# Kernel tuning notes

Hardware: AMD Instinct MI355X
Metric: run time of the kernel (lower is better)

## Reference

```python
import jax, jax.numpy as jnp
from jax import lax
import numpy as np

WINDOW_SIZE = 11
SIGMA = 1.5
C1 = 0.01 ** 2
C2 = 0.03 ** 2


def _gauss_1d(n=WINDOW_SIZE, sigma=SIGMA):
    # replicates cv2.getGaussianKernel(n, sigma)
    x = np.arange(n, dtype=np.float64) - (n - 1) / 2.0
    g = np.exp(-(x ** 2) / (2.0 * sigma ** 2))
    return (g / g.sum()).astype(np.float32)


def _blur(x, g):
    """Separable 2D Gaussian blur of x [N,1,H,W]; math equals conv with g g^T."""
    p = g.shape[0] // 2
    kh = g.reshape(1, 1, -1, 1).astype(x.dtype)  # [O,I,KH,1]
    kw = g.reshape(1, 1, 1, -1).astype(x.dtype)  # [O,I,1,KW]
    dn = ('NCHW', 'OIHW', 'NCHW')
    x = lax.conv_general_dilated(x, kh, (1, 1), [(p, p), (0, 0)], dimension_numbers=dn)
    x = lax.conv_general_dilated(x, kw, (1, 1), [(0, 0), (p, p)], dimension_numbers=dn)
    return x


def _ssim_loss_2d(a, b):
    """a, b: [N,1,H,W]. Returns 1 - mean(SSIM map) with the module's exact formula."""
    g = jnp.asarray(_gauss_1d())
    mu1 = _blur(a, g)
    mu2 = _blur(b, g)
    mu1_sq = mu1 * mu1
    mu2_sq = mu2 * mu2
    mu1_mu2 = mu1 * mu2
    sigma1_sq = _blur(a * a, g) - mu1_sq
    sigma2_sq = _blur(b * b, g) - mu2_sq
    sigma12 = _blur(a * b, g) - mu1_mu2
    luminance = (2 * mu1_mu2 + C1) / (mu1_sq + mu2_sq + C1)
    contrast = (2 * sigma12 + C2) / (sigma1_sq + sigma2_sq + C2)
    structure = (sigma12 + C2) / (jnp.sqrt(sigma1_sq) * jnp.sqrt(sigma2_sq) + C2)
    ssim = luminance * contrast * structure
    return 1.0 - ssim.mean()


def setup_inputs() -> dict:
    key = jax.random.key(0)
    k1, k2, k3 = jax.random.split(key, 3)
    img1_3d = jax.random.uniform(k1, (4, 1, 16, 512, 512), dtype=jnp.float32)
    img1_2d = jax.random.uniform(k2, (4, 1, 512, 512), dtype=jnp.float32)
    img2 = jax.random.uniform(k3, (4, 1, 16, 512, 512), dtype=jnp.float32)
    return {"img1_3d": img1_3d, "img1_2d": img1_2d, "img2": img2}


def reference(img1_3d, img1_2d, img2):
    B, C, D, H, W = img1_3d.shape  # C == 1 (forced by groups=C with single-out-channel weight)
    # 3D SSIM: kernel depth 1, depth padding 0 -> per-slice 2D blur; fold D into batch.
    a3 = img1_3d.reshape(B * D, 1, H, W)
    b3 = img2.reshape(B * D, 1, H, W)
    loss3d = _ssim_loss_2d(a3, b3)
    # 2D SSIM against depth-averaged img2.
    b2 = jnp.mean(img2, axis=2)  # [B,1,H,W]
    loss2d = _ssim_loss_2d(img1_2d, b2)
    return loss3d + loss2d
```

## Files before the change

kernel.cpp:

```cpp
#include <hip/hip_runtime.h>
#include <cmath>


#define WSZ 11
#define IMG 512
#define SLICE (IMG * IMG)

typedef float f32x2 __attribute__((ext_vector_type(2)));
typedef float f32x4 __attribute__((ext_vector_type(4)));

struct G11 { float w[WSZ]; };

__device__ __forceinline__ void row_barrier()
{
    asm volatile("s_waitcnt lgkmcnt(0)" ::: "memory");
    __builtin_amdgcn_s_barrier();
}

__global__ __launch_bounds__(256, 5)
void ssim_pk_kernel(const float* __restrict__ A3, const float* __restrict__ B3,
                    const float* __restrict__ A2, const float* __restrict__ B2,
                    double* __restrict__ acc, G11 gw)
{
    __shared__ f32x4 A4[2][262];
    __shared__ f32x4 B4[2][262];
    __shared__ f32x2 Z2[2][262];
    __shared__ float bsum[4];

    const int tx = threadIdx.x;
    const int x0 = tx * 2;

    const int unit = blockIdx.x;
    const float* Ap;
    const float* Bp;
    double* accp;
    int y0, TST;
    if (unit < 1536) {
        int slice = unit / 24;
        int band  = unit - slice * 24;
        Ap = A3 + (long)slice * SLICE;
        Bp = B3 + (long)slice * SLICE;
        accp = acc + 0;
        if (band < 16) { y0 = band * 22;              TST = 22 + 10; }
        else           { y0 = 352 + (band - 16) * 20; TST = 20 + 10; }
    } else {
        int uu = unit - 1536;
        int img  = uu >> 6;
        int band = uu & 63;
        Ap = A2 + (long)img * SLICE;
        Bp = B2 + (long)img * SLICE;
        accp = acc + 1;
        y0 = band * 8;
        TST = 8 + 10;
    }

    if (tx < 3) {
        f32x4 z4 = {0.f, 0.f, 0.f, 0.f};
        f32x2 z2 = {0.f, 0.f};
        A4[0][tx] = z4; A4[1][tx] = z4; A4[0][259 + tx] = z4; A4[1][259 + tx] = z4;
        B4[0][tx] = z4; B4[1][tx] = z4; B4[0][259 + tx] = z4; B4[1][259 + tx] = z4;
        Z2[0][tx] = z2; Z2[1][tx] = z2; Z2[0][259 + tx] = z2; Z2[1][259 + tx] = z2;
    }

    f32x2 ra[11], rb[11];
    #pragma unroll
    for (int i = 0; i < 11; i++) { ra[i] = (f32x2){0.f, 0.f}; rb[i] = (f32x2){0.f, 0.f}; }

    float sum = 0.f;

    f32x2 aN = {0.f, 0.f}, bN = {0.f, 0.f};
    {
        int r = y0 - 5;
        if (r >= 0 && r < IMG) {
            aN = *(const f32x2*)&Ap[(long)r * IMG + x0];
            bN = *(const f32x2*)&Bp[(long)r * IMG + x0];
        }
    }

    const f32x2 C1v = {1e-4f, 1e-4f};
    const f32x2 C2v = {9e-4f, 9e-4f};

    for (int t0 = 0; t0 < TST; t0 += 11) {
        #pragma unroll
        for (int u = 0; u < 11; u++) {
            const int t = t0 + u;
            if (t < TST) {
                ra[u] = aN;
                rb[u] = bN;

                {
                    int rn = y0 - 4 + t;
                    aN = (f32x2){0.f, 0.f}; bN = (f32x2){0.f, 0.f};
                    if ((t + 1 < TST) && rn >= 0 && rn < IMG) {
                        aN = *(const f32x2*)&Ap[(long)rn * IMG + x0];
                        bN = *(const f32x2*)&Bp[(long)rn * IMG + x0];
                    }
                }

                if (t >= 10) {
                    f32x2 m1 = {0.f, 0.f}, m2 = m1, xx = m1, yy = m1, zz = m1;
                    #pragma unroll
                    for (int j = 0; j < 11; j++) {
                        const int s = (u + 1 + j) % 11;
                        const f32x2 g2 = {gw.w[j], gw.w[j]};
                        f32x2 a = ra[s], b = rb[s];
                        f32x2 ga = g2 * a, gb = g2 * b;
                        m1 += ga; m2 += gb;
                        xx += ga * a; yy += gb * b; zz += ga * b;
                    }
                    const int buf = t & 1;
                    A4[buf][3 + tx] = __builtin_shufflevector(m1, m2, 0, 1, 2, 3);
                    B4[buf][3 + tx] = __builtin_shufflevector(xx, yy, 0, 1, 2, 3);
                    Z2[buf][3 + tx] = zz;
                    row_barrier();

                    f32x2 OM1 = {0.f, 0.f}, OM2 = OM1, OXX = OM1, OYY = OM1, OZZ = OM1;
                    {
                        f32x4 pa = A4[buf][tx], pb = B4[buf][tx];
                        f32x2 pz = Z2[buf][tx];
                        const f32x2 c = {gw.w[0], 0.f};
                        OM1 += c * __builtin_shufflevector(pa, pa, 1, 1);
                        OM2 += c * __builtin_shufflevector(pa, pa, 3, 3);
                        OXX += c * __builtin_shufflevector(pb, pb, 1, 1);
                        OYY += c * __builtin_shufflevector(pb, pb, 3, 3);
                        OZZ += c * __builtin_shufflevector(pz, pz, 1, 1);
                    }
                    #pragma unroll
                    for (int jj = 1; jj <= 5; jj++) {
                        f32x4 pa = A4[buf][tx + jj], pb = B4[buf][tx + jj];
                        f32x2 pz = Z2[buf][tx + jj];
                        const f32x2 cA = {gw.w[2 * jj - 1], gw.w[2 * jj - 2]};
                        const f32x2 cB = {gw.w[2 * jj],     gw.w[2 * jj - 1]};
                        OM1 += cA * __builtin_shufflevector(pa, pa, 0, 0)
                             + cB * __builtin_shufflevector(pa, pa, 1, 1);
                        OM2 += cA * __builtin_shufflevector(pa, pa, 2, 2)
                             + cB * __builtin_shufflevector(pa, pa, 3, 3);
                        OXX += cA * __builtin_shufflevector(pb, pb, 0, 0)
                             + cB * __builtin_shufflevector(pb, pb, 1, 1);
                        OYY += cA * __builtin_shufflevector(pb, pb, 2, 2)
                             + cB * __builtin_shufflevector(pb, pb, 3, 3);
                        OZZ += cA * __builtin_shufflevector(pz, pz, 0, 0)
                             + cB * __builtin_shufflevector(pz, pz, 1, 1);
                    }
                    {
                        f32x4 pa = A4[buf][tx + 6], pb = B4[buf][tx + 6];
                        f32x2 pz = Z2[buf][tx + 6];
                        const f32x2 c = {0.f, gw.w[10]};
                        OM1 += c * __builtin_shufflevector(pa, pa, 0, 0);
                        OM2 += c * __builtin_shufflevector(pa, pa, 2, 2);
                        OXX += c * __builtin_shufflevector(pb, pb, 0, 0);
                        OYY += c * __builtin_shufflevector(pb, pb, 2, 2);
                        OZZ += c * __builtin_shufflevector(pz, pz, 0, 0);
                    }

                    f32x2 m1s = OM1 * OM1, m2s = OM2 * OM2, m12 = OM1 * OM2;
                    f32x2 s1 = OXX - m1s, s2 = OYY - m2s, s12 = OZZ - m12;
                    f32x2 d1 = m1s + m2s + C1v;
                    f32x2 d2 = s1 + s2 + C2v;
                    f32x2 num = (2.f * m12 + C1v) * (2.f * s12 + C2v) * (s12 + C2v);
                    float d3x = __builtin_amdgcn_sqrtf(s1.x) * __builtin_amdgcn_sqrtf(s2.x) + 9e-4f;
                    float d3y = __builtin_amdgcn_sqrtf(s1.y) * __builtin_amdgcn_sqrtf(s2.y) + 9e-4f;
                    sum += num.x * __builtin_amdgcn_rcpf(d1.x * d2.x * d3x);
                    sum += num.y * __builtin_amdgcn_rcpf(d1.y * d2.y * d3y);
                }
            }
        }
    }

    for (int off = 32; off > 0; off >>= 1)
        sum += __shfl_down(sum, off, 64);
    if ((tx & 63) == 0) bsum[tx >> 6] = sum;
    __syncthreads();
    if (tx == 0) {
        float tot = bsum[0] + bsum[1] + bsum[2] + bsum[3];
        atomicAdd(accp, (double)tot);
    }
}

__global__ __launch_bounds__(256) void depth_mean4_kernel(
    const float4* __restrict__ img2, float4* __restrict__ b2)
{
    const int per = SLICE / 4;
    int idx = blockIdx.x * 256 + threadIdx.x;
    int b = idx >> 16;
    int p = idx & (per - 1);
    const float4* src = img2 + (long)b * 16 * per + p;
    float sx = 0.f, sy = 0.f, sz = 0.f, sw = 0.f;
    #pragma unroll
    for (int d = 0; d < 16; d++) {
        float4 v = src[(long)d * per];
        sx += v.x; sy += v.y; sz += v.z; sw += v.w;
    }
    float4 o; o.x = sx * 0.0625f; o.y = sy * 0.0625f; o.z = sz * 0.0625f; o.w = sw * 0.0625f;
    b2[idx] = o;
}

__global__ void finalize_kernel(const double* __restrict__ acc, float* __restrict__ out)
{
    double loss3 = 1.0 - acc[0] / (64.0 * (double)SLICE);
    double loss2 = 1.0 - acc[1] / (4.0 * (double)SLICE);
    out[0] = (float)(loss3 + loss2);
}

extern "C" void kernel_launch(void* const* d_in, const int* in_sizes, int n_in,
                              void* d_out, int out_size, void* d_ws, size_t ws_size,
                              hipStream_t stream)
{
    const float* img1_3d = (const float*)d_in[0];
    const float* img1_2d = (const float*)d_in[1];
    const float* img2    = (const float*)d_in[2];
    float* out = (float*)d_out;

    double* acc = (double*)d_ws;
    float*  b2  = (float*)((char*)d_ws + 256);

    G11 gw;
    {
        double g[WSZ], s = 0.0;
        for (int i = 0; i < WSZ; i++) {
            double xx = (double)i - (WSZ - 1) / 2.0;
            g[i] = std::exp(-(xx * xx) / (2.0 * 1.5 * 1.5));
            s += g[i];
        }
        for (int i = 0; i < WSZ; i++) gw.w[i] = (float)(g[i] / s);
    }

    hipMemsetAsync(acc, 0, 2 * sizeof(double), stream);

    depth_mean4_kernel<<<(4 * SLICE / 4) / 256, 256, 0, stream>>>(
        (const float4*)img2, (float4*)b2);

    ssim_pk_kernel<<<1792, 256, 0, stream>>>(img1_3d, img2, img1_2d, b2, acc, gw);

    finalize_kernel<<<1, 1, 0, stream>>>(acc, out);
}
```

Before: 105.4 us.

## Process two output rows per barrier with a 12-slot ring and quad LDS buffers

Restructures the sliding-window loop so each iteration loads two new input rows, computes two vertical blur passes into separate LDS buffers, and then does a single barrier before two horizontal passes. The register ring grows from 11 to 12 entries, the LDS staging goes from double to quad buffering, and the warm-up now loads the first 10 rows up front instead of looping through them with predicated compute. The goal is to halve the number of workgroup barriers per output row and to keep more loads in flight. In exchange it uses more registers and LDS, and the occupancy hint drops from 5 to 4 waves.

After: 93.98 us, median of 2. 1.12x faster.

```diff
diff --git a/kernel.cpp b/kernel.cpp
--- a/kernel.cpp
+++ b/kernel.cpp
@@ -17,14 +17,14 @@
     __builtin_amdgcn_s_barrier();
 }
 
-__global__ __launch_bounds__(256, 5)
+__global__ __launch_bounds__(256, 4)
 void ssim_pk_kernel(const float* __restrict__ A3, const float* __restrict__ B3,
                     const float* __restrict__ A2, const float* __restrict__ B2,
                     double* __restrict__ acc, G11 gw)
 {
-    __shared__ f32x4 A4[2][262];
-    __shared__ f32x4 B4[2][262];
-    __shared__ f32x2 Z2[2][262];
+    __shared__ f32x4 A4[4][262];
+    __shared__ f32x4 B4[4][262];
+    __shared__ f32x2 Z2[4][262];
     __shared__ float bsum[4];
 
     const int tx = threadIdx.x;
@@ -34,15 +34,15 @@
     const float* Ap;
     const float* Bp;
     double* accp;
-    int y0, TST;
+    int y0, BAND;
     if (unit < 1536) {
         int slice = unit / 24;
         int band  = unit - slice * 24;
         Ap = A3 + (long)slice * SLICE;
         Bp = B3 + (long)slice * SLICE;
         accp = acc + 0;
-        if (band < 16) { y0 = band * 22;              TST = 22 + 10; }
-        else           { y0 = 352 + (band - 16) * 20; TST = 20 + 10; }
+        if (band < 16) { y0 = band * 22;              BAND = 22; }
+        else           { y0 = 352 + (band - 16) * 20; BAND = 20; }
     } else {
         int uu = unit - 1536;
         int img  = uu >> 6;
@@ -51,118 +51,142 @@
         Bp = B2 + (long)img * SLICE;
         accp = acc + 1;
         y0 = band * 8;
-        TST = 8 + 10;
-    }
+        BAND = 8;
+    }
+    const int ITER = BAND >> 1;
 
     if (tx < 3) {
         f32x4 z4 = {0.f, 0.f, 0.f, 0.f};
         f32x2 z2 = {0.f, 0.f};
-        A4[0][tx] = z4; A4[1][tx] = z4; A4[0][259 + tx] = z4; A4[1][259 + tx] = z4;
-        B4[0][tx] = z4; B4[1][tx] = z4; B4[0][259 + tx] = z4; B4[1][259 + tx] = z4;
-        Z2[0][tx] = z2; Z2[1][tx] = z2; Z2[0][259 + tx] = z2; Z2[1][259 + tx] = z2;
-    }
-
-    f32x2 ra[11], rb[11];
-    #pragma unroll
-    for (int i = 0; i < 11; i++) { ra[i] = (f32x2){0.f, 0.f}; rb[i] = (f32x2){0.f, 0.f}; }
+        #pragma unroll
+        for (int b = 0; b < 4; b++) {
+            A4[b][tx] = z4; A4[b][259 + tx] = z4;
+            B4[b][tx] = z4; B4[b][259 + tx] = z4;
+            Z2[b][tx] = z2; Z2[b][259 + tx] = z2;
+        }
+    }
+
+    f32x2 ra[12], rb[12];
 
     float sum = 0.f;
-
-    f32x2 aN = {0.f, 0.f}, bN = {0.f, 0.f};
-    {
-        int r = y0 - 5;
-        if (r >= 0 && r < IMG) {
-            aN = *(const f32x2*)&Ap[(long)r * IMG + x0];
-            bN = *(const f32x2*)&Bp[(long)r * IMG + x0];
-        }
-    }
-
     const f32x2 C1v = {1e-4f, 1e-4f};
     const f32x2 C2v = {9e-4f, 9e-4f};
 
-    for (int t0 = 0; t0 < TST; t0 += 11) {
-        #pragma unroll
-        for (int u = 0; u < 11; u++) {
-            const int t = t0 + u;
-            if (t < TST) {
-                ra[u] = aN;
-                rb[u] = bN;
+    #pragma unroll
+    for (int t = 0; t < 10; t++) {
+        int r = y0 - 5 + t;
+        f32x2 a = {0.f, 0.f}, b = {0.f, 0.f};
+        if (r >= 0) {
+            a = *(const f32x2*)&Ap[(long)r * IMG + x0];
+            b = *(const f32x2*)&Bp[(long)r * IMG + x0];
+        }
+        ra[t] = a; rb[t] = b;
+    }
+    ra[10] = (f32x2){0.f, 0.f}; rb[10] = (f32x2){0.f, 0.f};
+    ra[11] = (f32x2){0.f, 0.f}; rb[11] = (f32x2){0.f, 0.f};
+
+    f32x2 aN0 = {0.f, 0.f}, bN0 = aN0, aN1 = aN0, bN1 = aN0;
+    {
+        int r0 = y0 + 5, r1 = y0 + 6;
+        if (r0 < IMG) { aN0 = *(const f32x2*)&Ap[(long)r0 * IMG + x0];
+                        bN0 = *(const f32x2*)&Bp[(long)r0 * IMG + x0]; }
+        if (r1 < IMG) { aN1 = *(const f32x2*)&Ap[(long)r1 * IMG + x0];
+                        bN1 = *(const f32x2*)&Bp[(long)r1 * IMG + x0]; }
+    }
+
+    auto vpass = [&](int base, int buf) {
+        f32x2 m1 = {0.f, 0.f}, m2 = m1, xx = m1, yy = m1, zz = m1;
+        #pragma unroll
+        for (int j = 0; j < 11; j++) {
+            const int s = (base + j) % 12;
+            const f32x2 g2 = {gw.w[j], gw.w[j]};
+            f32x2 a = ra[s], b = rb[s];
+            f32x2 ga = g2 * a, gb = g2 * b;
+            m1 += ga; m2 += gb;
+            xx += ga * a; yy += gb * b; zz += ga * b;
+        }
+        A4[buf][3 + tx] = __builtin_shufflevector(m1, m2, 0, 1, 2, 3);
+        B4[buf][3 + tx] = __builtin_shufflevector(xx, yy, 0, 1, 2, 3);
+        Z2[buf][3 + tx] = zz;
+    };
+
+    auto hpass = [&](int buf) {
+        f32x2 OM1 = {0.f, 0.f}, OM2 = OM1, OXX = OM1, OYY = OM1, OZZ = OM1;
+        {
+            f32x4 pa = A4[buf][tx], pb = B4[buf][tx];
+            f32x2 pz = Z2[buf][tx];
+            const f32x2 c = {gw.w[0], 0.f};
+            OM1 += c * __builtin_shufflevector(pa, pa, 1, 1);
+            OM2 += c * __builtin_shufflevector(pa, pa, 3, 3);
+            OXX += c * __builtin_shufflevector(pb, pb, 1, 1);
+            OYY += c * __builtin_shufflevector(pb, pb, 3, 3);
+            OZZ += c * __builtin_shufflevector(pz, pz, 1, 1);
+        }
+        #pragma unroll
+        for (int jj = 1; jj <= 5; jj++) {
+            f32x4 pa = A4[buf][tx + jj], pb = B4[buf][tx + jj];
+            f32x2 pz = Z2[buf][tx + jj];
+            const f32x2 cA = {gw.w[2 * jj - 1], gw.w[2 * jj - 2]};
+            const f32x2 cB = {gw.w[2 * jj],     gw.w[2 * jj - 1]};
+            OM1 += cA * __builtin_shufflevector(pa, pa, 0, 0)
+                 + cB * __builtin_shufflevector(pa, pa, 1, 1);
+            OM2 += cA * __builtin_shufflevector(pa, pa, 2, 2)
+                 + cB * __builtin_shufflevector(pa, pa, 3, 3);
+            OXX += cA * __builtin_shufflevector(pb, pb, 0, 0)
+                 + cB * __builtin_shufflevector(pb, pb, 1, 1);
+            OYY += cA * __builtin_shufflevector(pb, pb, 2, 2)
+                 + cB * __builtin_shufflevector(pb, pb, 3, 3);
+            OZZ += cA * __builtin_shufflevector(pz, pz, 0, 0)
+                 + cB * __builtin_shufflevector(pz, pz, 1, 1);
+        }
+        {
+            f32x4 pa = A4[buf][tx + 6], pb = B4[buf][tx + 6];
+            f32x2 pz = Z2[buf][tx + 6];
+            const f32x2 c = {0.f, gw.w[10]};
+            OM1 += c * __builtin_shufflevector(pa, pa, 0, 0);
+            OM2 += c * __builtin_shufflevector(pa, pa, 2, 2);
+            OXX += c * __builtin_shufflevector(pb, pb, 0, 0);
+            OYY += c * __builtin_shufflevector(pb, pb, 2, 2);
+            OZZ += c * __builtin_shufflevector(pz, pz, 0, 0);
+        }
+        f32x2 m1s = OM1 * OM1, m2s = OM2 * OM2, m12 = OM1 * OM2;
+        f32x2 s1 = OXX - m1s, s2 = OYY - m2s, s12 = OZZ - m12;
+        f32x2 d1 = m1s + m2s + C1v;
+        f32x2 d2 = s1 + s2 + C2v;
+        f32x2 num = (2.f * m12 + C1v) * (2.f * s12 + C2v) * (s12 + C2v);
+        float d3x = __builtin_amdgcn_sqrtf(s1.x) * __builtin_amdgcn_sqrtf(s2.x) + 9e-4f;
+        float d3y = __builtin_amdgcn_sqrtf(s1.y) * __builtin_amdgcn_sqrtf(s2.y) + 9e-4f;
+        sum += num.x * __builtin_amdgcn_rcpf(d1.x * d2.x * d3x);
+        sum += num.y * __builtin_amdgcn_rcpf(d1.y * d2.y * d3y);
+    };
+
+    for (int kk = 0; kk < ITER; kk += 6) {
+        #pragma unroll
+        for (int u = 0; u < 6; u++) {
+            const int k = kk + u;
+            if (k < ITER) {
+                const int s0 = (10 + 2 * u) % 12;
+                const int s1 = (11 + 2 * u) % 12;
+                ra[s0] = aN0; rb[s0] = bN0;
+                ra[s1] = aN1; rb[s1] = bN1;
 
                 {
-                    int rn = y0 - 4 + t;
-                    aN = (f32x2){0.f, 0.f}; bN = (f32x2){0.f, 0.f};
-                    if ((t + 1 < TST) && rn >= 0 && rn < IMG) {
-                        aN = *(const f32x2*)&Ap[(long)rn * IMG + x0];
-                        bN = *(const f32x2*)&Bp[(long)rn * IMG + x0];
+                    int r0 = y0 + 7 + 2 * k, r1 = r0 + 1;
+                    aN0 = (f32x2){0.f, 0.f}; bN0 = aN0; aN1 = aN0; bN1 = aN0;
+                    if (k + 1 < ITER) {
+                        if (r0 < IMG) { aN0 = *(const f32x2*)&Ap[(long)r0 * IMG + x0];
+                                        bN0 = *(const f32x2*)&Bp[(long)r0 * IMG + x0]; }
+                        if (r1 < IMG) { aN1 = *(const f32x2*)&Ap[(long)r1 * IMG + x0];
+                                        bN1 = *(const f32x2*)&Bp[(long)r1 * IMG + x0]; }
                     }
                 }
 
-                if (t >= 10) {
-                    f32x2 m1 = {0.f, 0.f}, m2 = m1, xx = m1, yy = m1, zz = m1;
-                    #pragma unroll
-                    for (int j = 0; j < 11; j++) {
-                        const int s = (u + 1 + j) % 11;
-                        const f32x2 g2 = {gw.w[j], gw.w[j]};
-                        f32x2 a = ra[s], b = rb[s];
-                        f32x2 ga = g2 * a, gb = g2 * b;
-                        m1 += ga; m2 += gb;
-                        xx += ga * a; yy += gb * b; zz += ga * b;
-                    }
-                    const int buf = t & 1;
-                    A4[buf][3 + tx] = __builtin_shufflevector(m1, m2, 0, 1, 2, 3);
-                    B4[buf][3 + tx] = __builtin_shufflevector(xx, yy, 0, 1, 2, 3);
-                    Z2[buf][3 + tx] = zz;
-                    row_barrier();
-
-                    f32x2 OM1 = {0.f, 0.f}, OM2 = OM1, OXX = OM1, OYY = OM1, OZZ = OM1;
-                    {
-                        f32x4 pa = A4[buf][tx], pb = B4[buf][tx];
-                        f32x2 pz = Z2[buf][tx];
-                        const f32x2 c = {gw.w[0], 0.f};
-                        OM1 += c * __builtin_shufflevector(pa, pa, 1, 1);
-                        OM2 += c * __builtin_shufflevector(pa, pa, 3, 3);
-                        OXX += c * __builtin_shufflevector(pb, pb, 1, 1);
-                        OYY += c * __builtin_shufflevector(pb, pb, 3, 3);
-                        OZZ += c * __builtin_shufflevector(pz, pz, 1, 1);
-                    }
-                    #pragma unroll
-                    for (int jj = 1; jj <= 5; jj++) {
-                        f32x4 pa = A4[buf][tx + jj], pb = B4[buf][tx + jj];
-                        f32x2 pz = Z2[buf][tx + jj];
-                        const f32x2 cA = {gw.w[2 * jj - 1], gw.w[2 * jj - 2]};
-                        const f32x2 cB = {gw.w[2 * jj],     gw.w[2 * jj - 1]};
-                        OM1 += cA * __builtin_shufflevector(pa, pa, 0, 0)
-                             + cB * __builtin_shufflevector(pa, pa, 1, 1);
-                        OM2 += cA * __builtin_shufflevector(pa, pa, 2, 2)
-                             + cB * __builtin_shufflevector(pa, pa, 3, 3);
-                        OXX += cA * __builtin_shufflevector(pb, pb, 0, 0)
-                             + cB * __builtin_shufflevector(pb, pb, 1, 1);
-                        OYY += cA * __builtin_shufflevector(pb, pb, 2, 2)
-                             + cB * __builtin_shufflevector(pb, pb, 3, 3);
-                        OZZ += cA * __builtin_shufflevector(pz, pz, 0, 0)
-                             + cB * __builtin_shufflevector(pz, pz, 1, 1);
-                    }
-                    {
-                        f32x4 pa = A4[buf][tx + 6], pb = B4[buf][tx + 6];
-                        f32x2 pz = Z2[buf][tx + 6];
-                        const f32x2 c = {0.f, gw.w[10]};
-                        OM1 += c * __builtin_shufflevector(pa, pa, 0, 0);
-                        OM2 += c * __builtin_shufflevector(pa, pa, 2, 2);
-                        OXX += c * __builtin_shufflevector(pb, pb, 0, 0);
-                        OYY += c * __builtin_shufflevector(pb, pb, 2, 2);
-                        OZZ += c * __builtin_shufflevector(pz, pz, 0, 0);
-                    }
-
-                    f32x2 m1s = OM1 * OM1, m2s = OM2 * OM2, m12 = OM1 * OM2;
-                    f32x2 s1 = OXX - m1s, s2 = OYY - m2s, s12 = OZZ - m12;
-                    f32x2 d1 = m1s + m2s + C1v;
-                    f32x2 d2 = s1 + s2 + C2v;
-                    f32x2 num = (2.f * m12 + C1v) * (2.f * s12 + C2v) * (s12 + C2v);
-                    float d3x = __builtin_amdgcn_sqrtf(s1.x) * __builtin_amdgcn_sqrtf(s2.x) + 9e-4f;
-                    float d3y = __builtin_amdgcn_sqrtf(s1.y) * __builtin_amdgcn_sqrtf(s2.y) + 9e-4f;
-                    sum += num.x * __builtin_amdgcn_rcpf(d1.x * d2.x * d3x);
-                    sum += num.y * __builtin_amdgcn_rcpf(d1.y * d2.y * d3y);
-                }
+                const int b0 = (u & 1) * 2;
+                vpass(2 * u,     b0);
+                vpass(2 * u + 1, b0 + 1);
+                row_barrier();
+                hpass(b0);
+                hpass(b0 + 1);
             }
         }
     }
```
